# Kernel tuning notes

Measured on AMD Instinct MI355X. Metric: run time of the kernel, lower is better.

The kernel has to match this reference:

```python
import jax, jax.numpy as jnp
import numpy as np

NUM_NETS = 262144
PINS_PER_NET = 4
NUM_PINS = NUM_NETS * PINS_PER_NET
NBX, NBY = 256, 256
XL, XH, YL, YH = 0.0, 512.0, 0.0, 512.0
BSX = (XH - XL) / NBX
BSY = (YH - YL) / NBY

# RISA wiring-distribution weight table, indexed by pin count (clamped at 46).
_RISA_TAB = jnp.asarray(np.array(
    [1.0, 1.0, 1.0, 1.0,
     1.0828, 1.1536, 1.2206, 1.2823, 1.3385, 1.3991, 1.4493]
    + [1.6899] * 5 + [1.8924] * 5 + [2.0743] * 5 + [2.2334] * 5
    + [2.3892] * 5 + [2.5356] * 5 + [2.6625] * 5 + [2.7933],
    dtype=np.float32))


def setup_inputs() -> dict:
    key = jax.random.key(0)
    k1, k2 = jax.random.split(key)
    # pin positions, interleaved xyxy..., uniform inside the layout region
    pin_pos = jax.random.uniform(k1, (2 * NUM_PINS,), jnp.float32, XL, XH)
    # CSR offsets: 4 pins per net (ragged structure handled generically below)
    netpin_start = jnp.arange(NUM_NETS + 1, dtype=jnp.int32) * PINS_PER_NET
    # flat net->pin map: a permutation of all pin ids
    flat_netpin = jax.random.permutation(k2, jnp.arange(NUM_PINS, dtype=jnp.int32))
    net_weights = jnp.ones((NUM_NETS,), jnp.float32)
    return {"pin_pos": pin_pos, "netpin_start": netpin_start,
            "flat_netpin": flat_netpin, "net_weights": net_weights}


def _net_density(pin_pos, netpin_start, flat_netpin, net_weights):
    num_nets = netpin_start.shape[0] - 1
    num_pins = flat_netpin.shape[0]
    # pin i (in flat order) belongs to net n with netpin_start[n] <= i < netpin_start[n+1]
    pin2net = jnp.searchsorted(netpin_start,
                               jnp.arange(num_pins, dtype=netpin_start.dtype),
                               side='right') - 1
    px = pin_pos[2 * flat_netpin]
    py = pin_pos[2 * flat_netpin + 1]
    # per-net bounding boxes via segment max/min
    x_max = jax.ops.segment_max(px, pin2net, num_segments=num_nets)
    x_min = -jax.ops.segment_max(-px, pin2net, num_segments=num_nets)
    y_max = jax.ops.segment_max(py, pin2net, num_segments=num_nets)
    y_min = -jax.ops.segment_max(-py, pin2net, num_segments=num_nets)
    # RISA weight from pin count, times the net weight
    cnt = netpin_start[1:] - netpin_start[:-1]
    wt = _RISA_TAB[jnp.minimum(cnt, _RISA_TAB.shape[0] - 1)] * net_weights
    # per-bin overlap lengths (separable in x and y): [num_nets, NBX] / [num_nets, NBY]
    bxl = XL + BSX * jnp.arange(NBX, dtype=pin_pos.dtype)
    byl = YL + BSY * jnp.arange(NBY, dtype=pin_pos.dtype)
    ox = jnp.clip(jnp.minimum(x_max[:, None], bxl + BSX) - jnp.maximum(x_min[:, None], bxl), 0.0)
    oy = jnp.clip(jnp.minimum(y_max[:, None], byl + BSY) - jnp.maximum(y_min[:, None], byl), 0.0)
    dx = x_max - x_min
    dy = y_max - y_min
    # horizontal demand ~ wt/dy, vertical demand ~ wt/dx (guard degenerate bboxes)
    ch = jnp.where(dy > 0, wt / jnp.maximum(dy, 1e-12), 0.0)
    cv = jnp.where(dx > 0, wt / jnp.maximum(dx, 1e-12), 0.0)
    # scatter-add over bins expressed as a dense contraction over nets
    H = jnp.einsum('nx,ny->xy', ch[:, None] * ox, oy)
    V = jnp.einsum('nx,ny->xy', cv[:, None] * ox, oy)
    return jnp.abs(H) + jnp.abs(V), H, V


def reference(pin_pos, netpin_start, flat_netpin, net_weights):
    return _net_density(pin_pos, netpin_start, flat_netpin, net_weights)
```

## Files before the change

kernel.cpp:

```cpp
#include <hip/hip_runtime.h>


#define NBX 256
#define NBY 256
#define CELLS (NBX * NBY)
#define STRIPS 16
#define SROWS 16
#define HALF_TILE (SROWS * NBY)
#define TILE_FLOATS (HALF_TILE * 2)
#define NSCAT 512
#define TOTAL_ENT 724992

#define BS_ 2.0f
#define INV_BS 0.5f

__constant__ float c_risa[47] = {
    1.0f, 1.0f, 1.0f, 1.0f,
    1.0828f, 1.1536f, 1.2206f, 1.2823f, 1.3385f, 1.3991f, 1.4493f,
    1.6899f, 1.6899f, 1.6899f, 1.6899f, 1.6899f,
    1.8924f, 1.8924f, 1.8924f, 1.8924f, 1.8924f,
    2.0743f, 2.0743f, 2.0743f, 2.0743f, 2.0743f,
    2.2334f, 2.2334f, 2.2334f, 2.2334f, 2.2334f,
    2.3892f, 2.3892f, 2.3892f, 2.3892f, 2.3892f,
    2.5356f, 2.5356f, 2.5356f, 2.5356f, 2.5356f,
    2.6625f, 2.6625f, 2.6625f, 2.6625f, 2.6625f,
    2.7933f};

__constant__ int c_bcnt[STRIPS] = {58,48,39,31,25,21,18,16,
                                   16,18,21,25,31,39,48,58};
__constant__ int c_boff[STRIPS + 1] = {0,58,106,145,176,201,222,240,256,
                                       272,290,311,336,367,406,454,512};
__constant__ int c_cap[STRIPS] = {81920,67584,54272,44032,35840,29696,25600,23552,
                                  23552,25600,29696,35840,44032,54272,67584,81920};
__constant__ int c_loff[STRIPS] = {0,81920,149504,203776,247808,283648,313344,338944,
                                   362496,386048,411648,441344,477184,521216,575488,643072};

__device__ __forceinline__ unsigned enc_x(float v) {
    float r = rintf(v * 8192.0f);
    r = fminf(fmaxf(r, 0.0f), 4194303.0f);
    return (unsigned)r;
}
__device__ __forceinline__ unsigned enc_y(float v) {
    float r = rintf(v * 128.0f);
    r = fminf(fmaxf(r, 0.0f), 65535.0f);
    return (unsigned)r;
}

__global__ void zero_cursors(int* __restrict__ cursors) {
    if (threadIdx.x < STRIPS) cursors[threadIdx.x] = 0;
}

__global__ __launch_bounds__(256) void bbox_lists(
        const float* __restrict__ pin_pos,
        const int* __restrict__ netpin_start,
        const int* __restrict__ flat_netpin,
        const float* __restrict__ net_weights,
        int4* __restrict__ list, int* __restrict__ cursors, int num_nets) {
    __shared__ int cnt[STRIPS];
    __shared__ int base_[STRIPS];
    int tid = threadIdx.x;
    if (tid < STRIPS) cnt[tid] = 0;
    __syncthreads();

    int n = blockIdx.x * 256 + tid;
    int st0 = -1, st1 = -1, st2 = -1, st3 = -1;
    int p0 = 0, p1 = 0, p2 = 0, p3 = 0;
    int4 r0 = make_int4(0, 0, 0, 0), r1 = make_int4(0, 0, 0, 0);
    if (n < num_nets) {
        int s = netpin_start[n];
        int e = netpin_start[n + 1];
        int pc = e - s;
        float xmin, xmax, ymin, ymax;
        if (pc == 4 && (s & 3) == 0) {
            int4 pid = *reinterpret_cast<const int4*>(flat_netpin + s);
            float2 q0 = *reinterpret_cast<const float2*>(pin_pos + 2 * (size_t)pid.x);
            float2 q1 = *reinterpret_cast<const float2*>(pin_pos + 2 * (size_t)pid.y);
            float2 q2 = *reinterpret_cast<const float2*>(pin_pos + 2 * (size_t)pid.z);
            float2 q3 = *reinterpret_cast<const float2*>(pin_pos + 2 * (size_t)pid.w);
            xmin = fminf(fminf(q0.x, q1.x), fminf(q2.x, q3.x));
            xmax = fmaxf(fmaxf(q0.x, q1.x), fmaxf(q2.x, q3.x));
            ymin = fminf(fminf(q0.y, q1.y), fminf(q2.y, q3.y));
            ymax = fmaxf(fmaxf(q0.y, q1.y), fmaxf(q2.y, q3.y));
        } else {
            xmin = 1e30f; xmax = -1e30f; ymin = 1e30f; ymax = -1e30f;
            for (int i = s; i < e; ++i) {
                int p = flat_netpin[i];
                float2 xy = *reinterpret_cast<const float2*>(pin_pos + 2 * (long)p);
                xmin = fminf(xmin, xy.x);
                xmax = fmaxf(xmax, xy.x);
                ymin = fminf(ymin, xy.y);
                ymax = fmaxf(ymax, xy.y);
            }
        }
        if (pc > 0) {
            float wt = c_risa[min(pc, 46)] * net_weights[n];
            float dx = xmax - xmin;
            float dy = ymax - ymin;
            float ch = (dy > 0.0f) ? wt / fmaxf(dy, 1e-12f) : 0.0f;
            float cv = (dx > 0.0f) ? wt / fmaxf(dx, 1e-12f) : 0.0f;
            if (ch != 0.0f || cv != 0.0f) {
                unsigned xf1 = enc_x(xmin), xf2 = enc_x(xmax);
                unsigned ypk = enc_y(ymin) | (enc_y(ymax) << 16);
                r0 = make_int4((int)xf1, (int)ypk, __float_as_int(ch), __float_as_int(cv));
                r1 = make_int4((int)xf2, (int)ypk, __float_as_int(-ch), __float_as_int(-cv));
                int k1 = xf1 >> 14;
                int k2 = xf2 >> 14;
                if (k1 < 256) {
                    st0 = k1 >> 4;
                    p0 = atomicAdd(&cnt[st0], 1);
                    int kb = k1 + 1;
                    if (kb < 256 && (kb >> 4) != st0) { st1 = kb >> 4; p1 = atomicAdd(&cnt[st1], 1); }
                }
                if (k2 < 256) {
                    st2 = k2 >> 4;
                    p2 = atomicAdd(&cnt[st2], 1);
                    int kb = k2 + 1;
                    if (kb < 256 && (kb >> 4) != st2) { st3 = kb >> 4; p3 = atomicAdd(&cnt[st3], 1); }
                }
            }
        }
    }
    __syncthreads();
    if (tid < STRIPS) base_[tid] = cnt[tid] ? atomicAdd(&cursors[tid], cnt[tid]) : 0;
    __syncthreads();
    if (st0 >= 0) { int pos = base_[st0] + p0; if (pos < c_cap[st0]) list[c_loff[st0] + pos] = r0; }
    if (st1 >= 0) { int pos = base_[st1] + p1; if (pos < c_cap[st1]) list[c_loff[st1] + pos] = r0; }
    if (st2 >= 0) { int pos = base_[st2] + p2; if (pos < c_cap[st2]) list[c_loff[st2] + pos] = r1; }
    if (st3 >= 0) { int pos = base_[st3] + p3; if (pos < c_cap[st3]) list[c_loff[st3] + pos] = r1; }
}

__global__ __launch_bounds__(512) void strip_scatter(
        const int4* __restrict__ list, const int* __restrict__ cursors,
        float* __restrict__ P) {
    __shared__ float lds[TILE_FLOATS];
    int bid = blockIdx.x;
    int strip = 0;
#pragma unroll
    for (int s = 1; s < STRIPS; ++s)
        if (bid >= c_boff[s]) strip = s;
    int sub = bid - c_boff[strip];
    int nb = c_bcnt[strip];
    int lo = strip * SROWS;
    int tid = threadIdx.x;
    float4* z = (float4*)lds;
    for (int j = tid; j < TILE_FLOATS / 4; j += 512) z[j] = make_float4(0, 0, 0, 0);
    __syncthreads();

    int len = min(cursors[strip], c_cap[strip]);
    const int4* A = list + c_loff[strip];
    int chunk = (len + nb - 1) / nb;
    int i0 = sub * chunk;
    int i1 = min(i0 + chunk, len);
    for (int i = i0 + tid; i < i1; i += 512) {
        int4 a = A[i];
        unsigned xf = (unsigned)a.x;
        int k = xf >> 14;
        float f = (float)(xf & 16383) * (1.0f / 16384.0f);
        int ks = (int)((xf + 8192u) >> 14);
        unsigned yp = (unsigned)a.y;
        unsigned y1 = yp & 0xffffu, y2 = yp >> 16;
        int j1 = (int)(y1 >> 8);
        float g1 = (float)(y1 & 255u) * (1.0f / 256.0f);
        int j2 = (int)(y2 >> 8);
        float g2 = (float)(y2 & 255u) * (1.0f / 256.0f);
        int js1 = (int)((y1 + 128u) >> 8);
        int js2 = (int)((y2 + 128u) >> 8);
        float sch = __int_as_float(a.z);
        float scv = __int_as_float(a.w);

        int rh = ks - lo;
        if ((unsigned)rh < SROWS) {
            float w = sch * (BS_ * BS_);
            int rbase = rh * NBY;
            if (j1 < NBY)     atomicAdd(&lds[rbase + j1],      w * (1.0f - g1));
            if (j1 + 1 < NBY) atomicAdd(&lds[rbase + j1 + 1],  w * g1);
            if (j2 < NBY)     atomicAdd(&lds[rbase + j2],     -w * (1.0f - g2));
            if (j2 + 1 < NBY) atomicAdd(&lds[rbase + j2 + 1], -w * g2);
        }
        if (js1 != js2) {
            float wv = scv * (BS_ * BS_);
            float w0 = wv * (1.0f - f);
            float w1 = wv * f;
#pragma unroll
            for (int r = 0; r < 2; ++r) {
                int rr = k + r - lo;
                if ((unsigned)rr >= SROWS) continue;
                float w = r ? w1 : w0;
                int rbase = HALF_TILE + rr * NBY;
                if (js1 < NBY) atomicAdd(&lds[rbase + js1],  w);
                if (js2 < NBY) atomicAdd(&lds[rbase + js2], -w);
            }
        }
    }
    __syncthreads();
    float4* dst = (float4*)(P + (size_t)bid * TILE_FLOATS);
    const float4* src = (const float4*)lds;
    for (int j = tid; j < TILE_FLOATS / 4; j += 512) dst[j] = src[j];
}

__global__ void merge_scany(const float* __restrict__ P, float2* __restrict__ T) {
    __shared__ float sh[256];
    __shared__ float sv[256];
    int x = blockIdx.x;
    int t = threadIdx.x;
    int strip = x >> 4;
    int r = x & 15;
    int b0 = c_boff[strip], b1 = c_boff[strip + 1];
    const float* base = P + (size_t)b0 * TILE_FLOATS + r * NBY + t;
    float h = 0.0f, v = 0.0f;
    for (int b = b0; b < b1; ++b) {
        h += base[0];
        v += base[HALF_TILE];
        base += TILE_FLOATS;
    }
    sh[t] = h; sv[t] = v;
    __syncthreads();
    for (int off = 1; off < 256; off <<= 1) {
        float ah = (t >= off) ? sh[t - off] : 0.0f;
        float av = (t >= off) ? sv[t - off] : 0.0f;
        __syncthreads();
        sh[t] += ah;
        sv[t] += av;
        __syncthreads();
    }
    T[x * NBY + t] = make_float2(sh[t], sv[t]);
}

__global__ void scanx_out(const float2* __restrict__ T, float* __restrict__ out) {
    __shared__ float sh[256];
    __shared__ float sv[256];
    int y = blockIdx.x;
    int t = threadIdx.x;
    float2 c = T[t * NBY + y];
    sh[t] = c.x; sv[t] = c.y;
    __syncthreads();
    for (int off = 1; off < 256; off <<= 1) {
        float ah = (t >= off) ? sh[t - off] : 0.0f;
        float av = (t >= off) ? sv[t - off] : 0.0f;
        __syncthreads();
        sh[t] += ah;
        sv[t] += av;
        __syncthreads();
    }
    float h = sh[t], v = sv[t];
    int idx = t * NBY + y;
    out[idx] = fabsf(h) + fabsf(v);
    out[CELLS + idx] = h;
    out[2 * CELLS + idx] = v;
}

__global__ void zero_dense(float* __restrict__ S) {
    int i = blockIdx.x * blockDim.x + threadIdx.x;
    if (i < CELLS * 2) S[i] = 0.0f;
}

__global__ void fused_atomic(const float* __restrict__ pin_pos,
                             const int* __restrict__ netpin_start,
                             const int* __restrict__ flat_netpin,
                             const float* __restrict__ net_weights,
                             float* __restrict__ S, int num_nets) {
    int n = blockIdx.x * blockDim.x + threadIdx.x;
    if (n >= num_nets) return;
    int s = netpin_start[n];
    int e = netpin_start[n + 1];
    int pc = e - s;
    if (pc <= 0) return;
    float xmin = 1e30f, xmax = -1e30f, ymin = 1e30f, ymax = -1e30f;
    for (int i = s; i < e; ++i) {
        int p = flat_netpin[i];
        float2 xy = *reinterpret_cast<const float2*>(pin_pos + 2 * (long)p);
        xmin = fminf(xmin, xy.x);
        xmax = fmaxf(xmax, xy.x);
        ymin = fminf(ymin, xy.y);
        ymax = fmaxf(ymax, xy.y);
    }
    float wt = c_risa[min(pc, 46)] * net_weights[n];
    float dx = xmax - xmin;
    float dy = ymax - ymin;
    float ch = (dy > 0.0f) ? wt / fmaxf(dy, 1e-12f) : 0.0f;
    float cv = (dx > 0.0f) ? wt / fmaxf(dx, 1e-12f) : 0.0f;
    if (ch == 0.0f && cv == 0.0f) return;
    float t1 = xmin * INV_BS, t2 = xmax * INV_BS;
    int k1 = min(max((int)floorf(t1), 0), 256);
    int k2 = min(max((int)floorf(t2), 0), 256);
    float fx1 = t1 - k1, fx2 = t2 - k2;
    float u1 = ymin * INV_BS, u2 = ymax * INV_BS;
    int j1 = min(max((int)floorf(u1), 0), 256);
    int j2 = min(max((int)floorf(u2), 0), 256);
    float fy1 = u1 - j1, fy2 = u2 - j2;
    int   xi[4] = {k1, k1 + 1, k2, k2 + 1};
    float xw[4] = {BS_ * (1 - fx1), BS_ * fx1, -BS_ * (1 - fx2), -BS_ * fx2};
    int   yi[4] = {j1, j1 + 1, j2, j2 + 1};
    float yw[4] = {BS_ * (1 - fy1), BS_ * fy1, -BS_ * (1 - fy2), -BS_ * fy2};
#pragma unroll
    for (int a = 0; a < 4; ++a) {
        if (xi[a] >= NBX) continue;
        int rbase = xi[a] * NBY;
        float wh = ch * xw[a];
        float wv = cv * xw[a];
#pragma unroll
        for (int b = 0; b < 4; ++b) {
            if (yi[b] >= NBY) continue;
            int off = rbase + yi[b];
            atomicAdd(&S[off], wh * yw[b]);
            atomicAdd(&S[off + CELLS], wv * yw[b]);
        }
    }
}

__global__ void scany_dense(const float* __restrict__ S, float2* __restrict__ T) {
    __shared__ float sh[256];
    __shared__ float sv[256];
    int x = blockIdx.x;
    int t = threadIdx.x;
    sh[t] = S[x * NBY + t];
    sv[t] = S[CELLS + x * NBY + t];
    __syncthreads();
    for (int off = 1; off < 256; off <<= 1) {
        float ah = (t >= off) ? sh[t - off] : 0.0f;
        float av = (t >= off) ? sv[t - off] : 0.0f;
        __syncthreads();
        sh[t] += ah;
        sv[t] += av;
        __syncthreads();
    }
    T[x * NBY + t] = make_float2(sh[t], sv[t]);
}

static inline size_t alignup(size_t v, size_t a) { return (v + a - 1) & ~(a - 1); }

extern "C" void kernel_launch(void* const* d_in, const int* in_sizes, int n_in,
                              void* d_out, int out_size, void* d_ws, size_t ws_size,
                              hipStream_t stream) {
    const float* pin_pos = (const float*)d_in[0];
    const int* netpin_start = (const int*)d_in[1];
    const int* flat_netpin = (const int*)d_in[2];
    const float* net_weights = (const float*)d_in[3];
    int num_nets = in_sizes[1] - 1;

    size_t off = 0;
    size_t list_off = off; off = alignup(off + (size_t)TOTAL_ENT * 16, 16);
    size_t P_off = off;    off = alignup(off + (size_t)NSCAT * TILE_FLOATS * 4, 16);
    size_t T_off = off;    off = alignup(off + (size_t)CELLS * 8, 16);
    size_t cur_off = off;  off += 256;
    size_t need = off;

    float* out = (float*)d_out;
    char* ws = (char*)d_ws;
    int nb = (num_nets + 255) / 256;

    if (ws_size >= need && num_nets <= 262144) {
        int4* list = (int4*)(ws + list_off);
        float* P = (float*)(ws + P_off);
        float2* T = (float2*)(ws + T_off);
        int* cursors = (int*)(ws + cur_off);
        zero_cursors<<<1, 64, 0, stream>>>(cursors);
        bbox_lists<<<nb, 256, 0, stream>>>(pin_pos, netpin_start, flat_netpin,
                                           net_weights, list, cursors, num_nets);
        strip_scatter<<<NSCAT, 512, 0, stream>>>(list, cursors, P);
        merge_scany<<<NBX, 256, 0, stream>>>(P, T);
        scanx_out<<<NBY, 256, 0, stream>>>(T, out);
    } else {
        float* S = (float*)ws;
        float2* T = (float2*)(ws + (size_t)CELLS * 2 * sizeof(float));
        zero_dense<<<(CELLS * 2 + 255) / 256, 256, 0, stream>>>(S);
        fused_atomic<<<nb, 256, 0, stream>>>(pin_pos, netpin_start, flat_netpin,
                                             net_weights, S, num_nets);
        scany_dense<<<NBX, 256, 0, stream>>>(S, T);
        scanx_out<<<NBY, 256, 0, stream>>>(T, out);
    }
}
```

Before: 84.22 us.

## Fuse all pipeline stages into one cooperative kernel with grid syncs

Replaces the five separate kernel launches (zero cursors, bbox lists, strip scatter, merge/scan-y, scan-x) with a single cooperative kernel of 512 blocks that separates the stages with grid.sync(). The aim is to remove per-launch overhead and the idle gaps between dependent kernels. The bbox stage now handles 512 nets per block instead of 256, so 512 blocks cover all nets. In exchange, the later scan stages leave many blocks and threads idle, and each grid-wide barrier adds its own cost. It falls back to the old multi-kernel path if the cooperative launch fails.

```diff
diff --git a/kernel.cpp b/kernel.cpp
--- a/kernel.cpp
+++ b/kernel.cpp
@@ -1,4 +1,7 @@
 #include <hip/hip_runtime.h>
+#include <hip/hip_cooperative_groups.h>
+
+namespace cg = cooperative_groups;
 
 
 #define NBX 256
@@ -46,6 +49,215 @@
     return (unsigned)r;
 }
 
+__global__ __launch_bounds__(512) void fused_all(
+        const float* __restrict__ pin_pos,
+        const int* __restrict__ netpin_start,
+        const int* __restrict__ flat_netpin,
+        const float* __restrict__ net_weights,
+        int4* __restrict__ list, int* __restrict__ cursors,
+        float* __restrict__ P, float2* __restrict__ T,
+        float* __restrict__ out, int num_nets) {
+    cg::grid_group grid = cg::this_grid();
+    __shared__ float lds[TILE_FLOATS];
+    int bid = blockIdx.x;
+    int tid = threadIdx.x;
+
+    if (bid == 0 && tid < STRIPS) cursors[tid] = 0;
+    grid.sync();
+
+    {
+        int* cnt = (int*)lds;
+        int* base_ = cnt + STRIPS;
+        if (tid < STRIPS) cnt[tid] = 0;
+        __syncthreads();
+        int n = bid * 512 + tid;
+        int st0 = -1, st1 = -1, st2 = -1, st3 = -1;
+        int p0 = 0, p1 = 0, p2 = 0, p3 = 0;
+        int4 r0 = make_int4(0, 0, 0, 0), r1 = make_int4(0, 0, 0, 0);
+        if (n < num_nets) {
+            int s = netpin_start[n];
+            int e = netpin_start[n + 1];
+            int pc = e - s;
+            float xmin, xmax, ymin, ymax;
+            if (pc == 4 && (s & 3) == 0) {
+                int4 pid = *reinterpret_cast<const int4*>(flat_netpin + s);
+                float2 q0 = *reinterpret_cast<const float2*>(pin_pos + 2 * (size_t)pid.x);
+                float2 q1 = *reinterpret_cast<const float2*>(pin_pos + 2 * (size_t)pid.y);
+                float2 q2 = *reinterpret_cast<const float2*>(pin_pos + 2 * (size_t)pid.z);
+                float2 q3 = *reinterpret_cast<const float2*>(pin_pos + 2 * (size_t)pid.w);
+                xmin = fminf(fminf(q0.x, q1.x), fminf(q2.x, q3.x));
+                xmax = fmaxf(fmaxf(q0.x, q1.x), fmaxf(q2.x, q3.x));
+                ymin = fminf(fminf(q0.y, q1.y), fminf(q2.y, q3.y));
+                ymax = fmaxf(fmaxf(q0.y, q1.y), fmaxf(q2.y, q3.y));
+            } else {
+                xmin = 1e30f; xmax = -1e30f; ymin = 1e30f; ymax = -1e30f;
+                for (int i = s; i < e; ++i) {
+                    int p = flat_netpin[i];
+                    float2 xy = *reinterpret_cast<const float2*>(pin_pos + 2 * (long)p);
+                    xmin = fminf(xmin, xy.x);
+                    xmax = fmaxf(xmax, xy.x);
+                    ymin = fminf(ymin, xy.y);
+                    ymax = fmaxf(ymax, xy.y);
+                }
+            }
+            if (pc > 0) {
+                float wt = c_risa[min(pc, 46)] * net_weights[n];
+                float dx = xmax - xmin;
+                float dy = ymax - ymin;
+                float ch = (dy > 0.0f) ? wt / fmaxf(dy, 1e-12f) : 0.0f;
+                float cv = (dx > 0.0f) ? wt / fmaxf(dx, 1e-12f) : 0.0f;
+                if (ch != 0.0f || cv != 0.0f) {
+                    unsigned xf1 = enc_x(xmin), xf2 = enc_x(xmax);
+                    unsigned ypk = enc_y(ymin) | (enc_y(ymax) << 16);
+                    r0 = make_int4((int)xf1, (int)ypk, __float_as_int(ch), __float_as_int(cv));
+                    r1 = make_int4((int)xf2, (int)ypk, __float_as_int(-ch), __float_as_int(-cv));
+                    int k1 = xf1 >> 14;
+                    int k2 = xf2 >> 14;
+                    if (k1 < 256) {
+                        st0 = k1 >> 4;
+                        p0 = atomicAdd(&cnt[st0], 1);
+                        int kb = k1 + 1;
+                        if (kb < 256 && (kb >> 4) != st0) { st1 = kb >> 4; p1 = atomicAdd(&cnt[st1], 1); }
+                    }
+                    if (k2 < 256) {
+                        st2 = k2 >> 4;
+                        p2 = atomicAdd(&cnt[st2], 1);
+                        int kb = k2 + 1;
+                        if (kb < 256 && (kb >> 4) != st2) { st3 = kb >> 4; p3 = atomicAdd(&cnt[st3], 1); }
+                    }
+                }
+            }
+        }
+        __syncthreads();
+        if (tid < STRIPS) base_[tid] = cnt[tid] ? atomicAdd(&cursors[tid], cnt[tid]) : 0;
+        __syncthreads();
+        if (st0 >= 0) { int pos = base_[st0] + p0; if (pos < c_cap[st0]) list[c_loff[st0] + pos] = r0; }
+        if (st1 >= 0) { int pos = base_[st1] + p1; if (pos < c_cap[st1]) list[c_loff[st1] + pos] = r0; }
+        if (st2 >= 0) { int pos = base_[st2] + p2; if (pos < c_cap[st2]) list[c_loff[st2] + pos] = r1; }
+        if (st3 >= 0) { int pos = base_[st3] + p3; if (pos < c_cap[st3]) list[c_loff[st3] + pos] = r1; }
+    }
+    grid.sync();
+
+    {
+        int strip = 0;
+#pragma unroll
+        for (int s = 1; s < STRIPS; ++s)
+            if (bid >= c_boff[s]) strip = s;
+        int sub = bid - c_boff[strip];
+        int nb = c_bcnt[strip];
+        int lo = strip * SROWS;
+        float4* z = (float4*)lds;
+        for (int j = tid; j < TILE_FLOATS / 4; j += 512) z[j] = make_float4(0, 0, 0, 0);
+        __syncthreads();
+
+        int len = min(cursors[strip], c_cap[strip]);
+        const int4* A = list + c_loff[strip];
+        int chunk = (len + nb - 1) / nb;
+        int i0 = sub * chunk;
+        int i1 = min(i0 + chunk, len);
+        for (int i = i0 + tid; i < i1; i += 512) {
+            int4 a = A[i];
+            unsigned xf = (unsigned)a.x;
+            int k = xf >> 14;
+            float f = (float)(xf & 16383) * (1.0f / 16384.0f);
+            int ks = (int)((xf + 8192u) >> 14);
+            unsigned yp = (unsigned)a.y;
+            unsigned y1 = yp & 0xffffu, y2 = yp >> 16;
+            int j1 = (int)(y1 >> 8);
+            float g1 = (float)(y1 & 255u) * (1.0f / 256.0f);
+            int j2 = (int)(y2 >> 8);
+            float g2 = (float)(y2 & 255u) * (1.0f / 256.0f);
+            int js1 = (int)((y1 + 128u) >> 8);
+            int js2 = (int)((y2 + 128u) >> 8);
+            float sch = __int_as_float(a.z);
+            float scv = __int_as_float(a.w);
+
+            int rh = ks - lo;
+            if ((unsigned)rh < SROWS) {
+                float w = sch * (BS_ * BS_);
+                int rbase = rh * NBY;
+                if (j1 < NBY)     atomicAdd(&lds[rbase + j1],      w * (1.0f - g1));
+                if (j1 + 1 < NBY) atomicAdd(&lds[rbase + j1 + 1],  w * g1);
+                if (j2 < NBY)     atomicAdd(&lds[rbase + j2],     -w * (1.0f - g2));
+                if (j2 + 1 < NBY) atomicAdd(&lds[rbase + j2 + 1], -w * g2);
+            }
+            if (js1 != js2) {
+                float wv = scv * (BS_ * BS_);
+                float w0 = wv * (1.0f - f);
+                float w1 = wv * f;
+#pragma unroll
+                for (int r = 0; r < 2; ++r) {
+                    int rr = k + r - lo;
+                    if ((unsigned)rr >= SROWS) continue;
+                    float w = r ? w1 : w0;
+                    int rbase = HALF_TILE + rr * NBY;
+                    if (js1 < NBY) atomicAdd(&lds[rbase + js1],  w);
+                    if (js2 < NBY) atomicAdd(&lds[rbase + js2], -w);
+                }
+            }
+        }
+        __syncthreads();
+        float4* dst = (float4*)(P + (size_t)bid * TILE_FLOATS);
+        const float4* src = (const float4*)lds;
+        for (int j = tid; j < TILE_FLOATS / 4; j += 512) dst[j] = src[j];
+    }
+    grid.sync();
+
+    {
+        float* sh = lds;
+        float* sv = lds + 256;
+        bool act = (bid < NBX) && (tid < 256);
+        if (act) {
+            int strip = bid >> 4;
+            int r = bid & 15;
+            int b0 = c_boff[strip], b1 = c_boff[strip + 1];
+            const float* base = P + (size_t)b0 * TILE_FLOATS + r * NBY + tid;
+            float h = 0.0f, v = 0.0f;
+            for (int b = b0; b < b1; ++b) {
+                h += base[0];
+                v += base[HALF_TILE];
+                base += TILE_FLOATS;
+            }
+            sh[tid] = h; sv[tid] = v;
+        }
+        __syncthreads();
+        for (int off = 1; off < 256; off <<= 1) {
+            float ah = 0.0f, av = 0.0f;
+            if (act && tid >= off) { ah = sh[tid - off]; av = sv[tid - off]; }
+            __syncthreads();
+            if (act) { sh[tid] += ah; sv[tid] += av; }
+            __syncthreads();
+        }
+        if (act) T[bid * NBY + tid] = make_float2(sh[tid], sv[tid]);
+    }
+    grid.sync();
+
+    {
+        float* sh = lds;
+        float* sv = lds + 256;
+        bool act = (bid < NBY) && (tid < 256);
+        if (act) {
+            float2 c = T[tid * NBY + bid];
+            sh[tid] = c.x; sv[tid] = c.y;
+        }
+        __syncthreads();
+        for (int off = 1; off < 256; off <<= 1) {
+            float ah = 0.0f, av = 0.0f;
+            if (act && tid >= off) { ah = sh[tid - off]; av = sv[tid - off]; }
+            __syncthreads();
+            if (act) { sh[tid] += ah; sv[tid] += av; }
+            __syncthreads();
+        }
+        if (act) {
+            float h = sh[tid], v = sv[tid];
+            int idx = tid * NBY + bid;
+            out[idx] = fabsf(h) + fabsf(v);
+            out[CELLS + idx] = h;
+            out[2 * CELLS + idx] = v;
+        }
+    }
+}
+
 __global__ void zero_cursors(int* __restrict__ cursors) {
     if (threadIdx.x < STRIPS) cursors[threadIdx.x] = 0;
 }
@@ -61,7 +273,6 @@
     int tid = threadIdx.x;
     if (tid < STRIPS) cnt[tid] = 0;
     __syncthreads();
-
     int n = blockIdx.x * 256 + tid;
     int st0 = -1, st1 = -1, st2 = -1, st3 = -1;
     int p0 = 0, p1 = 0, p2 = 0, p3 = 0;
@@ -145,7 +356,6 @@
     float4* z = (float4*)lds;
     for (int j = tid; j < TILE_FLOATS / 4; j += 512) z[j] = make_float4(0, 0, 0, 0);
     __syncthreads();
-
     int len = min(cursors[strip], c_cap[strip]);
     const int4* A = list + c_loff[strip];
     int chunk = (len + nb - 1) / nb;
@@ -167,7 +377,6 @@
         int js2 = (int)((y2 + 128u) >> 8);
         float sch = __int_as_float(a.z);
         float scv = __int_as_float(a.w);
-
         int rh = ks - lo;
         if ((unsigned)rh < SROWS) {
             float w = sch * (BS_ * BS_);
@@ -354,12 +563,23 @@
         float* P = (float*)(ws + P_off);
         float2* T = (float2*)(ws + T_off);
         int* cursors = (int*)(ws + cur_off);
-        zero_cursors<<<1, 64, 0, stream>>>(cursors);
-        bbox_lists<<<nb, 256, 0, stream>>>(pin_pos, netpin_start, flat_netpin,
-                                           net_weights, list, cursors, num_nets);
-        strip_scatter<<<NSCAT, 512, 0, stream>>>(list, cursors, P);
-        merge_scany<<<NBX, 256, 0, stream>>>(P, T);
-        scanx_out<<<NBY, 256, 0, stream>>>(T, out);
+
+        void* args[] = {(void*)&pin_pos, (void*)&netpin_start,
+                        (void*)&flat_netpin, (void*)&net_weights,
+                        (void*)&list, (void*)&cursors, (void*)&P, (void*)&T,
+                        (void*)&out, (void*)&num_nets};
+        hipError_t err = hipLaunchCooperativeKernel(
+            reinterpret_cast<const void*>(&fused_all),
+            dim3(NSCAT), dim3(512), args, 0, stream);
+        if (err != hipSuccess) {
+            zero_cursors<<<1, 64, 0, stream>>>(cursors);
+            bbox_lists<<<nb, 256, 0, stream>>>(pin_pos, netpin_start,
+                                               flat_netpin, net_weights, list,
+                                               cursors, num_nets);
+            strip_scatter<<<NSCAT, 512, 0, stream>>>(list, cursors, P);
+            merge_scany<<<NBX, 256, 0, stream>>>(P, T);
+            scanx_out<<<NBY, 256, 0, stream>>>(T, out);
+        }
     } else {
         float* S = (float*)ws;
         float2* T = (float2*)(ws + (size_t)CELLS * 2 * sizeof(float));
```

Result: slower. 285.0 us (+238.3%).
